# Performance work log

Measured on AMD Instinct MI355X. Metric: run time of the kernel, lower is better.

## Reference

```python
import jax, jax.numpy as jnp
import numpy as np

N = 262144   # number of units (batched instances of the module)
G = 128      # universe_field side length
D = 128      # dimension
RADIUS = 3   # min(3, G//2) == 3

# First D=128 neighborhood offsets in the original triple-loop order (i-major, j, k)
_grid = np.stack(np.meshgrid(np.arange(-RADIUS, RADIUS + 1),
                             np.arange(-RADIUS, RADIUS + 1),
                             np.arange(-RADIUS, RADIUS + 1), indexing='ij'), -1).reshape(-1, 3)[:D]
OI = jnp.asarray(_grid[:, 0], dtype=jnp.int32)
OJ = jnp.asarray(_grid[:, 1], dtype=jnp.int32)
OK = jnp.asarray(_grid[:, 2], dtype=jnp.int32)


def setup_inputs() -> dict:
    key = jax.random.key(0)
    ks = jax.random.split(key, 8)
    return {
        'universe_field': jax.random.normal(ks[0], (G, G, G), jnp.float32),
        'positions': jax.random.uniform(ks[1], (N, 3), jnp.float32) * G,
        'signatures': jax.random.normal(ks[2], (N, D), jnp.float32),
        'offsets': jax.random.normal(ks[3], (N, 3), jnp.float32) * 0.1,
        'W1': jax.random.normal(ks[4], (2 * D, D), jnp.float32) * (1.0 / np.sqrt(2 * D)),
        'b1': jax.random.normal(ks[5], (D,), jnp.float32) * 0.01,
        'W2': jax.random.normal(ks[6], (D, D), jnp.float32) * (1.0 / np.sqrt(D)),
        'b2': jax.random.normal(ks[7], (D,), jnp.float32) * 0.01,
    }


def _sample_local(field, pos):
    # pos: [N,3] float; truncate to int (torch .long()) then clamp, like the original
    pc = jnp.clip(jax.lax.stop_gradient(pos).astype(jnp.int32), 0, G - 1)  # [N,3]
    xx = jnp.clip(pc[:, 0:1] + OI[None, :], 0, G - 1)  # [N,D]
    yy = jnp.clip(pc[:, 1:2] + OJ[None, :], 0, G - 1)
    zz = jnp.clip(pc[:, 2:3] + OK[None, :], 0, G - 1)
    return field[xx, yy, zz]  # [N,D] gathered local field (343 points truncated to D)


def _stability(field, pos, signatures, W1, b1, W2, b2):
    local = _sample_local(field, pos)                       # [N,D]
    combined = jnp.concatenate([signatures, local], axis=-1)  # [N,2D]
    h = jnp.tanh(combined @ W1 + b1)                        # [N,D]
    resp = h @ W2 + b2                                      # [N,D]
    return jnp.linalg.norm(resp - signatures, axis=-1)      # [N]


def reference(universe_field, positions, signatures, offsets, W1, b1, W2, b2):
    stab_old = _stability(universe_field, positions, signatures, W1, b1, W2, b2)
    test_pos = positions + offsets
    stab_new = _stability(universe_field, test_pos, signatures, W1, b1, W2, b2)
    accept = stab_new <= stab_old                           # revert move if new_stab > old_stab
    final_pos = jnp.where(accept[:, None], test_pos, positions)
    stability = jnp.where(accept, stab_new, stab_old)
    return stability, final_pos
```

## Files before the change

kernel.cpp:

```cpp
#include <hip/hip_runtime.h>
#include <hip/hip_bf16.h>

#define NU 262144
#define GG 128
#define PG 134
#define DD 128

typedef __attribute__((ext_vector_type(8))) short short8;
typedef __attribute__((ext_vector_type(4))) float f32x4;

union Frag { short8 s; unsigned u[4]; };

__device__ __forceinline__ unsigned short f2b(float f) {
  union { float f; unsigned u; } v; v.f = f;
  unsigned r = v.u + 0x7fffu + ((v.u >> 16) & 1u);
  return (unsigned short)(r >> 16);
}
__device__ __forceinline__ unsigned cvtpk(float lo, float hi) {
  unsigned r;
  asm("v_cvt_pk_bf16_f32 %0, %1, %2" : "=v"(r) : "v"(lo), "v"(hi));
  return r;
}
__device__ __forceinline__ float unplo(unsigned w) {
  union { unsigned u; float f; } v; v.u = w << 16; return v.f;
}
__device__ __forceinline__ float unphi(unsigned w) {
  union { unsigned u; float f; } v; v.u = w & 0xffff0000u; return v.f;
}

__device__ __forceinline__ float fast_tanh(float x) {
  float e = __expf(fabsf(x) * 2.0f);
  float r = __frcp_rn(e + 1.0f);
  return copysignf(fmaf(-2.0f, r, 1.0f), x);
}

struct alignas(16) RowdT { int v[20]; };
static constexpr RowdT mkrowd() {
  RowdT t{};
  for (int r = 0; r < 20; ++r) {
    int rr = (r < 18) ? r : 18;
    int di = (rr < 18) ? (-3 + rr / 7) : -1;
    int dj = (rr < 18) ? (-3 + rr % 7) : 1;
    t.v[r] = (di * PG + dj) * PG - 3;
  }
  return t;
}
__device__ constexpr RowdT ROWD = mkrowd();

__global__ void prep_field(const float* __restrict__ f, unsigned short* __restrict__ fp) {
  int idx = blockIdx.x * 256 + threadIdx.x;
  if (idx >= PG * PG * PG) return;
  int z = idx % PG, t = idx / PG;
  int y = t % PG, x = t / PG;
  int xx = min(max(x - 3, 0), GG - 1);
  int yy = min(max(y - 3, 0), GG - 1);
  int zz = min(max(z - 3, 0), GG - 1);
  fp[idx] = f2b(f[(xx * GG + yy) * GG + zz]);
}

__global__ void prep_w(const float* __restrict__ W1, const float* __restrict__ W2,
                       unsigned short* __restrict__ wall) {
  int idx = blockIdx.x * 256 + threadIdx.x;
  if (idx >= 6656) return;
  int kt = idx >> 9, nt = (idx >> 6) & 7, ln = idx & 63;
  int n = nt * 16 + (ln & 15), lg = ln >> 4;
  short8 s;
  if (kt < 4) {
    int k0 = kt * 32 + lg * 8;
#pragma unroll
    for (int j = 0; j < 8; ++j) s[j] = (short)f2b(W1[(k0 + j) * DD + n]);
  } else if (kt < 9) {
    int r = (kt - 4) * 4 + lg;
#pragma unroll
    for (int j = 0; j < 8; ++j) {
      bool valid = (r < 18 && j < 7) || (r == 18 && j < 2);
      int row = 128 + ((r < 18) ? (r * 7 + j) : (126 + j));
      s[j] = valid ? (short)f2b(W1[row * DD + n]) : (short)0;
    }
  } else {
    int k0 = (kt - 9) * 32 + lg * 8;
#pragma unroll
    for (int j = 0; j < 8; ++j) s[j] = (short)f2b(W2[(k0 + j) * DD + n]);
  }
  ((short8*)wall)[idx] = s;
}

__global__ __launch_bounds__(512, 4) void atu_main(
    const float* __restrict__ pos, const float* __restrict__ sig,
    const float* __restrict__ offs,
    const float* __restrict__ b1, const float* __restrict__ b2,
    const unsigned short* __restrict__ fpad, const unsigned short* __restrict__ wall,
    float* __restrict__ out_stab, float* __restrict__ out_pos)
{
  __shared__ unsigned short ldsw[2][8192];
  __shared__ alignas(16) unsigned short ns[8][2048];
  const int tid  = threadIdx.x;
  const int lane = tid & 63;
  const int lg   = lane >> 4, lm = lane & 15;
  const int wid  = tid >> 6;
  int bid = blockIdx.x;
  int swz = (bid & 7) * 256 + (bid >> 3);
  const int ub = swz * 128 + wid * 16;
  const int un = ub + lm;
  char* nsb = (char*)&ns[wid][0];

  int abase[2];
  {
    float px = pos[un * 3 + 0], py = pos[un * 3 + 1], pz = pos[un * 3 + 2];
    float qx = px + offs[un * 3 + 0], qy = py + offs[un * 3 + 1], qz = pz + offs[un * 3 + 2];
    int ax = min(max((int)px, 0), GG - 1), ay = min(max((int)py, 0), GG - 1), az = min(max((int)pz, 0), GG - 1);
    int bx = min(max((int)qx, 0), GG - 1), by = min(max((int)qy, 0), GG - 1), bz = min(max((int)qz, 0), GG - 1);
    abase[0] = ((ax + 3) * PG + (ay + 3)) * PG + (az + 3);
    abase[1] = ((bx + 3) * PG + (by + 3)) * PG + (bz + 3);
  }

  const short8* wfr = (const short8*)wall;
  const char* fpadb = (const char*)fpad;

  f32x4 acc[8][2];
#pragma unroll
  for (int nt = 0; nt < 8; ++nt) { acc[nt][0] = f32x4{0.f,0.f,0.f,0.f}; acc[nt][1] = f32x4{0.f,0.f,0.f,0.f}; }
  f32x4 acc2[8][2];
  unsigned Q[2][8][2];

#define WRBUF(H, R0, R1)                                                        \
  *(short8*)((char*)&ldsw[H][0] + tid * 16) = (R0);                             \
  *(short8*)((char*)&ldsw[H][0] + 8192 + tid * 16) = (R1);

#define SIG_KT(KT, HALF)                                                        \
  {                                                                             \
    const f32x4* sp = (const f32x4*)(sig + (size_t)un * DD + (KT) * 32 + lg * 8); \
    f32x4 a = sp[0], b = sp[1];                                                 \
    Frag B;                                                                     \
    B.u[0] = cvtpk(a[0], a[1]); B.u[1] = cvtpk(a[2], a[3]);                     \
    B.u[2] = cvtpk(b[0], b[1]); B.u[3] = cvtpk(b[2], b[3]);                     \
     \
    *(short8*)(nsb + ((KT) * 4 + lg) * 256 + lm * 16) = B.s;                    \
    const char* buf = (const char*)&ldsw[HALF][0] + (((KT) & 1) ? 8192 : 0);    \
    _Pragma("unroll")                                                           \
    for (int nt = 0; nt < 8; ++nt) {                                            \
      short8 af = *(const short8*)(buf + (nt * 64 + lane) * 16);                \
      acc[nt][0] = __builtin_amdgcn_mfma_f32_16x16x32_bf16(af, B.s, acc[nt][0], 0, 0, 0); \
    }                                                                           \
  }

#define ROW_KT(KT, HALF)                                                        \
  {                                                                             \
    int rd = ROWD.v[((KT) - 4) * 4 + lg];                                       \
    short8 B0 = *(const short8*)(fpadb + 2 * (size_t)(abase[0] + rd));          \
    short8 B1 = *(const short8*)(fpadb + 2 * (size_t)(abase[1] + rd));          \
    const char* buf = (const char*)&ldsw[HALF][0] + (((KT) & 1) ? 8192 : 0);    \
    _Pragma("unroll")                                                           \
    for (int nt = 0; nt < 8; ++nt) {                                            \
      short8 af = *(const short8*)(buf + (nt * 64 + lane) * 16);                \
      acc[nt][0] = __builtin_amdgcn_mfma_f32_16x16x32_bf16(af, B0, acc[nt][0], 0, 0, 0); \
      acc[nt][1] = __builtin_amdgcn_mfma_f32_16x16x32_bf16(af, B1, acc[nt][1], 0, 0, 0); \
    }                                                                           \
  }

#define G2_KT(KT, HALF)                                                         \
  {                                                                             \
    constexpr int kb = (KT) - 9;                                                \
    Frag W[2];                                                                  \
    _Pragma("unroll")                                                           \
    for (int ut = 0; ut < 2; ++ut) {                                            \
      int qa0 = (int)Q[ut][2 * kb][0],     qa1 = (int)Q[ut][2 * kb][1];         \
      int qb0 = (int)Q[ut][2 * kb + 1][0], qb1 = (int)Q[ut][2 * kb + 1][1];     \
      int r00 = __builtin_amdgcn_ds_bpermute(ad0, qa0);                         \
      int r01 = __builtin_amdgcn_ds_bpermute(ad0, qa1);                         \
      int r10 = __builtin_amdgcn_ds_bpermute(ad1, qa0);                         \
      int r11 = __builtin_amdgcn_ds_bpermute(ad1, qa1);                         \
      int s00 = __builtin_amdgcn_ds_bpermute(ad0, qb0);                         \
      int s01 = __builtin_amdgcn_ds_bpermute(ad0, qb1);                         \
      int s10 = __builtin_amdgcn_ds_bpermute(ad1, qb0);                         \
      int s11 = __builtin_amdgcn_ds_bpermute(ad1, qb1);                         \
      W[ut].u[0] = (unsigned)(hi ? s00 : r00);                                  \
      W[ut].u[1] = (unsigned)(hi ? s01 : r01);                                  \
      W[ut].u[2] = (unsigned)(hi ? s10 : r10);                                  \
      W[ut].u[3] = (unsigned)(hi ? s11 : r11);                                  \
    }                                                                           \
    const char* buf = (const char*)&ldsw[HALF][0] + (((KT) & 1) ? 8192 : 0);    \
    _Pragma("unroll")                                                           \
    for (int nt = 0; nt < 8; ++nt) {                                            \
      short8 af = *(const short8*)(buf + (nt * 64 + lane) * 16);                \
      acc2[nt][0] = __builtin_amdgcn_mfma_f32_16x16x32_bf16(af, W[0].s, acc2[nt][0], 0, 0, 0); \
      acc2[nt][1] = __builtin_amdgcn_mfma_f32_16x16x32_bf16(af, W[1].s, acc2[nt][1], 0, 0, 0); \
    }                                                                           \
  }

  const int ad0 = ((((2 * lg) & 3) * 16) + lm) * 4;
  const int ad1 = ((((2 * lg + 1) & 3) * 16) + lm) * 4;
  const bool hi = (lg >= 2);

  short8 c0 = wfr[tid],        c1 = wfr[512 + tid];
  short8 n0 = wfr[1024 + tid], n1 = wfr[1536 + tid];
  WRBUF(0, c0, c1)
  __syncthreads();

  c0 = wfr[2048 + tid]; c1 = wfr[2560 + tid];
  SIG_KT(0, 0) SIG_KT(1, 0)
  WRBUF(1, n0, n1)
  __syncthreads();

  n0 = wfr[3072 + tid]; n1 = wfr[3584 + tid];
  SIG_KT(2, 1) SIG_KT(3, 1)
  WRBUF(0, c0, c1)
  __syncthreads();

#pragma unroll
  for (int nt = 0; nt < 8; ++nt) acc[nt][1] = acc[nt][0];

  c0 = wfr[4096 + tid]; c1 = wfr[4608 + tid];
  ROW_KT(4, 0) ROW_KT(5, 0)
  WRBUF(1, n0, n1)
  __syncthreads();

  n0 = wfr[5120 + tid]; n1 = wfr[5632 + tid];
  ROW_KT(6, 1) ROW_KT(7, 1)
  WRBUF(0, c0, c1)
  __syncthreads();

  c0 = wfr[6144 + tid];
  ROW_KT(8, 0)

#pragma unroll
  for (int nt = 0; nt < 8; ++nt) {
    f32x4 b1v = *(const f32x4*)(b1 + nt * 16 + lg * 4);
#pragma unroll
    for (int ut = 0; ut < 2; ++ut) {
      float h0 = fast_tanh(acc[nt][ut][0] + b1v[0]);
      float h1 = fast_tanh(acc[nt][ut][1] + b1v[1]);
      float h2 = fast_tanh(acc[nt][ut][2] + b1v[2]);
      float h3 = fast_tanh(acc[nt][ut][3] + b1v[3]);
      Q[ut][nt][0] = cvtpk(h0, h1);
      Q[ut][nt][1] = cvtpk(h2, h3);
    }
  }
#pragma unroll
  for (int nt = 0; nt < 8; ++nt) {
    f32x4 b2v = *(const f32x4*)(b2 + nt * 16 + lg * 4);
    acc2[nt][0] = b2v; acc2[nt][1] = b2v;
  }

  G2_KT(9, 0)
  WRBUF(1, n0, n1)
  __syncthreads();

  G2_KT(10, 1) G2_KT(11, 1)
  *(short8*)((char*)&ldsw[0][0] + tid * 16) = c0;
  __syncthreads();

  G2_KT(12, 0)

  float ssq[2] = {0.f, 0.f};
#pragma unroll
  for (int nt = 0; nt < 8; ++nt) {
    unsigned long long w64 = *(const unsigned long long*)
        (nsb + (nt * 2 + (lg >> 1)) * 256 + lm * 16 + (lg & 1) * 8);
    unsigned w0 = (unsigned)w64, w1 = (unsigned)(w64 >> 32);
    float sv0 = unplo(w0), sv1 = unphi(w0);
    float sv2 = unplo(w1), sv3 = unphi(w1);
#pragma unroll
    for (int ut = 0; ut < 2; ++ut) {
      float d0 = acc2[nt][ut][0] - sv0;
      float d1 = acc2[nt][ut][1] - sv1;
      float d2 = acc2[nt][ut][2] - sv2;
      float d3 = acc2[nt][ut][3] - sv3;
      ssq[ut] = fmaf(d0, d0, ssq[ut]);
      ssq[ut] = fmaf(d1, d1, ssq[ut]);
      ssq[ut] = fmaf(d2, d2, ssq[ut]);
      ssq[ut] = fmaf(d3, d3, ssq[ut]);
    }
  }
  ssq[0] += __shfl_xor(ssq[0], 16, 64); ssq[0] += __shfl_xor(ssq[0], 32, 64);
  ssq[1] += __shfl_xor(ssq[1], 16, 64); ssq[1] += __shfl_xor(ssq[1], 32, 64);

  if (lane < 16) {
    float px = pos[un * 3 + 0], py = pos[un * 3 + 1], pz = pos[un * 3 + 2];
    float ox = offs[un * 3 + 0], oy = offs[un * 3 + 1], oz = offs[un * 3 + 2];
    bool ok = ssq[1] <= ssq[0];
    out_stab[un] = sqrtf(ok ? ssq[1] : ssq[0]);
    out_pos[un * 3 + 0] = ok ? px + ox : px;
    out_pos[un * 3 + 1] = ok ? py + oy : py;
    out_pos[un * 3 + 2] = ok ? pz + oz : pz;
  }
#undef WRBUF
#undef SIG_KT
#undef ROW_KT
#undef G2_KT
}

extern "C" void kernel_launch(void* const* d_in, const int* in_sizes, int n_in,
                              void* d_out, int out_size, void* d_ws, size_t ws_size,
                              hipStream_t stream) {
  const float* field = (const float*)d_in[0];
  const float* pos   = (const float*)d_in[1];
  const float* sig   = (const float*)d_in[2];
  const float* offs  = (const float*)d_in[3];
  const float* W1    = (const float*)d_in[4];
  const float* b1    = (const float*)d_in[5];
  const float* W2    = (const float*)d_in[6];
  const float* b2    = (const float*)d_in[7];
  float* out_stab = (float*)d_out;
  float* out_pos  = out_stab + NU;

  char* ws = (char*)d_ws;
  unsigned short* fpad = (unsigned short*)ws;
  unsigned short* wall = (unsigned short*)(ws + 4812800);

  prep_field<<<(PG * PG * PG + 255) / 256, 256, 0, stream>>>(field, fpad);
  prep_w<<<26, 256, 0, stream>>>(W1, W2, wall);
  atu_main<<<NU / 128, 512, 0, stream>>>(pos, sig, offs, b1, b2,
                                         fpad, wall, out_stab, out_pos);
}
```

Measured before the change: 147.0 us.

## Stream weights via global_load_lds and software-prefetch signature and field fragments

After: 137.3 us. 1.07x faster.

```diff
diff --git a/kernel.cpp b/kernel.cpp
--- a/kernel.cpp
+++ b/kernel.cpp
@@ -103,6 +103,8 @@
   const int ub = swz * 128 + wid * 16;
   const int un = ub + lm;
   char* nsb = (char*)&ns[wid][0];
+  const char* wallb = (const char*)wall;
+  const char* fpadb = (const char*)fpad;
 
   int abase[2];
   {
@@ -114,124 +116,139 @@
     abase[1] = ((bx + 3) * PG + (by + 3)) * PG + (bz + 3);
   }
 
-  const short8* wfr = (const short8*)wall;
-  const char* fpadb = (const char*)fpad;
+#define GLL2(KTA, H)                                                              \
+  __builtin_amdgcn_global_load_lds(                                               \
+      (const unsigned*)(wallb + (((KTA) * 512 + tid) * 16)),                      \
+      (unsigned*)((char*)&ldsw[H][0] + wid * 1024), 16, 0, 0);                    \
+  __builtin_amdgcn_global_load_lds(                                               \
+      (const unsigned*)(wallb + ((((KTA) + 1) * 512 + tid) * 16)),                \
+      (unsigned*)((char*)&ldsw[H][0] + 8192 + wid * 1024), 16, 0, 0);
+
+#define GLL1(KTA, H)                                                              \
+  __builtin_amdgcn_global_load_lds(                                               \
+      (const unsigned*)(wallb + (((KTA) * 512 + tid) * 16)),                      \
+      (unsigned*)((char*)&ldsw[H][0] + wid * 1024), 16, 0, 0);
+
+  GLL2(0, 0)
+  f32x4 spa = *(const f32x4*)(sig + (size_t)un * DD + lg * 8);
+  f32x4 spb = *(const f32x4*)(sig + (size_t)un * DD + lg * 8 + 4);
+  short8 rAc, rBc;
+  {
+    int rd = ROWD.v[lg];
+    rAc = *(const short8*)(fpadb + 2 * (size_t)(abase[0] + rd));
+    rBc = *(const short8*)(fpadb + 2 * (size_t)(abase[1] + rd));
+  }
 
   f32x4 acc[8][2];
 #pragma unroll
-  for (int nt = 0; nt < 8; ++nt) { acc[nt][0] = f32x4{0.f,0.f,0.f,0.f}; acc[nt][1] = f32x4{0.f,0.f,0.f,0.f}; }
+  for (int nt = 0; nt < 8; ++nt) acc[nt][0] = *(const f32x4*)(b1 + nt * 16 + lg * 4);
   f32x4 acc2[8][2];
   unsigned Q[2][8][2];
 
-#define WRBUF(H, R0, R1)                                                        \
-  *(short8*)((char*)&ldsw[H][0] + tid * 16) = (R0);                             \
-  *(short8*)((char*)&ldsw[H][0] + 8192 + tid * 16) = (R1);
-
-#define SIG_KT(KT, HALF)                                                        \
-  {                                                                             \
-    const f32x4* sp = (const f32x4*)(sig + (size_t)un * DD + (KT) * 32 + lg * 8); \
-    f32x4 a = sp[0], b = sp[1];                                                 \
-    Frag B;                                                                     \
-    B.u[0] = cvtpk(a[0], a[1]); B.u[1] = cvtpk(a[2], a[3]);                     \
-    B.u[2] = cvtpk(b[0], b[1]); B.u[3] = cvtpk(b[2], b[3]);                     \
-     \
-    *(short8*)(nsb + ((KT) * 4 + lg) * 256 + lm * 16) = B.s;                    \
-    const char* buf = (const char*)&ldsw[HALF][0] + (((KT) & 1) ? 8192 : 0);    \
-    _Pragma("unroll")                                                           \
-    for (int nt = 0; nt < 8; ++nt) {                                            \
-      short8 af = *(const short8*)(buf + (nt * 64 + lane) * 16);                \
+  __syncthreads();
+
+#define SIG_KT(KT, HALF)                                                          \
+  {                                                                               \
+    f32x4 na, nb;                                                                 \
+    if ((KT) < 3) {                                                               \
+      na = *(const f32x4*)(sig + (size_t)un * DD + ((KT) + 1) * 32 + lg * 8);     \
+      nb = *(const f32x4*)(sig + (size_t)un * DD + ((KT) + 1) * 32 + lg * 8 + 4); \
+    }                                                                             \
+    Frag B;                                                                       \
+    B.u[0] = cvtpk(spa[0], spa[1]); B.u[1] = cvtpk(spa[2], spa[3]);               \
+    B.u[2] = cvtpk(spb[0], spb[1]); B.u[3] = cvtpk(spb[2], spb[3]);               \
+    *(short8*)(nsb + ((KT) * 4 + lg) * 256 + lm * 16) = B.s;                      \
+    const char* buf = (const char*)&ldsw[HALF][0] + (((KT) & 1) ? 8192 : 0);      \
+    _Pragma("unroll")                                                             \
+    for (int nt = 0; nt < 8; ++nt) {                                              \
+      short8 af = *(const short8*)(buf + (nt * 64 + lane) * 16);                  \
       acc[nt][0] = __builtin_amdgcn_mfma_f32_16x16x32_bf16(af, B.s, acc[nt][0], 0, 0, 0); \
-    }                                                                           \
-  }
-
-#define ROW_KT(KT, HALF)                                                        \
-  {                                                                             \
-    int rd = ROWD.v[((KT) - 4) * 4 + lg];                                       \
-    short8 B0 = *(const short8*)(fpadb + 2 * (size_t)(abase[0] + rd));          \
-    short8 B1 = *(const short8*)(fpadb + 2 * (size_t)(abase[1] + rd));          \
-    const char* buf = (const char*)&ldsw[HALF][0] + (((KT) & 1) ? 8192 : 0);    \
-    _Pragma("unroll")                                                           \
-    for (int nt = 0; nt < 8; ++nt) {                                            \
-      short8 af = *(const short8*)(buf + (nt * 64 + lane) * 16);                \
-      acc[nt][0] = __builtin_amdgcn_mfma_f32_16x16x32_bf16(af, B0, acc[nt][0], 0, 0, 0); \
-      acc[nt][1] = __builtin_amdgcn_mfma_f32_16x16x32_bf16(af, B1, acc[nt][1], 0, 0, 0); \
-    }                                                                           \
-  }
-
-#define G2_KT(KT, HALF)                                                         \
-  {                                                                             \
-    constexpr int kb = (KT) - 9;                                                \
-    Frag W[2];                                                                  \
-    _Pragma("unroll")                                                           \
-    for (int ut = 0; ut < 2; ++ut) {                                            \
-      int qa0 = (int)Q[ut][2 * kb][0],     qa1 = (int)Q[ut][2 * kb][1];         \
-      int qb0 = (int)Q[ut][2 * kb + 1][0], qb1 = (int)Q[ut][2 * kb + 1][1];     \
-      int r00 = __builtin_amdgcn_ds_bpermute(ad0, qa0);                         \
-      int r01 = __builtin_amdgcn_ds_bpermute(ad0, qa1);                         \
-      int r10 = __builtin_amdgcn_ds_bpermute(ad1, qa0);                         \
-      int r11 = __builtin_amdgcn_ds_bpermute(ad1, qa1);                         \
-      int s00 = __builtin_amdgcn_ds_bpermute(ad0, qb0);                         \
-      int s01 = __builtin_amdgcn_ds_bpermute(ad0, qb1);                         \
-      int s10 = __builtin_amdgcn_ds_bpermute(ad1, qb0);                         \
-      int s11 = __builtin_amdgcn_ds_bpermute(ad1, qb1);                         \
-      W[ut].u[0] = (unsigned)(hi ? s00 : r00);                                  \
-      W[ut].u[1] = (unsigned)(hi ? s01 : r01);                                  \
-      W[ut].u[2] = (unsigned)(hi ? s10 : r10);                                  \
-      W[ut].u[3] = (unsigned)(hi ? s11 : r11);                                  \
-    }                                                                           \
-    const char* buf = (const char*)&ldsw[HALF][0] + (((KT) & 1) ? 8192 : 0);    \
-    _Pragma("unroll")                                                           \
-    for (int nt = 0; nt < 8; ++nt) {                                            \
-      short8 af = *(const short8*)(buf + (nt * 64 + lane) * 16);                \
+    }                                                                             \
+    if ((KT) < 3) { spa = na; spb = nb; }                                         \
+  }
+
+#define ROW_KT(KT, HALF)                                                          \
+  {                                                                               \
+    short8 nA, nB;                                                                \
+    if ((KT) < 8) {                                                               \
+      int rn = ROWD.v[((KT) - 3) * 4 + lg];                                       \
+      nA = *(const short8*)(fpadb + 2 * (size_t)(abase[0] + rn));                 \
+      nB = *(const short8*)(fpadb + 2 * (size_t)(abase[1] + rn));                 \
+    }                                                                             \
+    const char* buf = (const char*)&ldsw[HALF][0] + (((KT) & 1) ? 8192 : 0);      \
+    _Pragma("unroll")                                                             \
+    for (int nt = 0; nt < 8; ++nt) {                                              \
+      short8 af = *(const short8*)(buf + (nt * 64 + lane) * 16);                  \
+      acc[nt][0] = __builtin_amdgcn_mfma_f32_16x16x32_bf16(af, rAc, acc[nt][0], 0, 0, 0); \
+      acc[nt][1] = __builtin_amdgcn_mfma_f32_16x16x32_bf16(af, rBc, acc[nt][1], 0, 0, 0); \
+    }                                                                             \
+    if ((KT) < 8) { rAc = nA; rBc = nB; }                                         \
+  }
+
+#define G2_KT(KT, HALF)                                                           \
+  {                                                                               \
+    constexpr int kb = (KT) - 9;                                                  \
+    Frag W[2];                                                                    \
+    _Pragma("unroll")                                                             \
+    for (int ut = 0; ut < 2; ++ut) {                                              \
+      int qa0 = (int)Q[ut][2 * kb][0],     qa1 = (int)Q[ut][2 * kb][1];           \
+      int qb0 = (int)Q[ut][2 * kb + 1][0], qb1 = (int)Q[ut][2 * kb + 1][1];       \
+      int r00 = __builtin_amdgcn_ds_bpermute(ad0, qa0);                           \
+      int r01 = __builtin_amdgcn_ds_bpermute(ad0, qa1);                           \
+      int r10 = __builtin_amdgcn_ds_bpermute(ad1, qa0);                           \
+      int r11 = __builtin_amdgcn_ds_bpermute(ad1, qa1);                           \
+      int s00 = __builtin_amdgcn_ds_bpermute(ad0, qb0);                           \
+      int s01 = __builtin_amdgcn_ds_bpermute(ad0, qb1);                           \
+      int s10 = __builtin_amdgcn_ds_bpermute(ad1, qb0);                           \
+      int s11 = __builtin_amdgcn_ds_bpermute(ad1, qb1);                           \
+      W[ut].u[0] = (unsigned)(hi ? s00 : r00);                                    \
+      W[ut].u[1] = (unsigned)(hi ? s01 : r01);                                    \
+      W[ut].u[2] = (unsigned)(hi ? s10 : r10);                                    \
+      W[ut].u[3] = (unsigned)(hi ? s11 : r11);                                    \
+    }                                                                             \
+    const char* buf = (const char*)&ldsw[HALF][0] + (((KT) & 1) ? 8192 : 0);      \
+    _Pragma("unroll")                                                             \
+    for (int nt = 0; nt < 8; ++nt) {                                              \
+      short8 af = *(const short8*)(buf + (nt * 64 + lane) * 16);                  \
       acc2[nt][0] = __builtin_amdgcn_mfma_f32_16x16x32_bf16(af, W[0].s, acc2[nt][0], 0, 0, 0); \
       acc2[nt][1] = __builtin_amdgcn_mfma_f32_16x16x32_bf16(af, W[1].s, acc2[nt][1], 0, 0, 0); \
-    }                                                                           \
+    }                                                                             \
   }
 
   const int ad0 = ((((2 * lg) & 3) * 16) + lm) * 4;
   const int ad1 = ((((2 * lg + 1) & 3) * 16) + lm) * 4;
   const bool hi = (lg >= 2);
 
-  short8 c0 = wfr[tid],        c1 = wfr[512 + tid];
-  short8 n0 = wfr[1024 + tid], n1 = wfr[1536 + tid];
-  WRBUF(0, c0, c1)
-  __syncthreads();
-
-  c0 = wfr[2048 + tid]; c1 = wfr[2560 + tid];
+  GLL2(2, 1)
   SIG_KT(0, 0) SIG_KT(1, 0)
-  WRBUF(1, n0, n1)
-  __syncthreads();
-
-  n0 = wfr[3072 + tid]; n1 = wfr[3584 + tid];
+  __syncthreads();
+
+  GLL2(4, 0)
   SIG_KT(2, 1) SIG_KT(3, 1)
-  WRBUF(0, c0, c1)
   __syncthreads();
 
 #pragma unroll
   for (int nt = 0; nt < 8; ++nt) acc[nt][1] = acc[nt][0];
 
-  c0 = wfr[4096 + tid]; c1 = wfr[4608 + tid];
+  GLL2(6, 1)
   ROW_KT(4, 0) ROW_KT(5, 0)
-  WRBUF(1, n0, n1)
-  __syncthreads();
-
-  n0 = wfr[5120 + tid]; n1 = wfr[5632 + tid];
+  __syncthreads();
+
+  GLL2(8, 0)
   ROW_KT(6, 1) ROW_KT(7, 1)
-  WRBUF(0, c0, c1)
-  __syncthreads();
-
-  c0 = wfr[6144 + tid];
+  __syncthreads();
+
+  GLL2(10, 1)
   ROW_KT(8, 0)
 
 #pragma unroll
   for (int nt = 0; nt < 8; ++nt) {
-    f32x4 b1v = *(const f32x4*)(b1 + nt * 16 + lg * 4);
 #pragma unroll
     for (int ut = 0; ut < 2; ++ut) {
-      float h0 = fast_tanh(acc[nt][ut][0] + b1v[0]);
-      float h1 = fast_tanh(acc[nt][ut][1] + b1v[1]);
-      float h2 = fast_tanh(acc[nt][ut][2] + b1v[2]);
-      float h3 = fast_tanh(acc[nt][ut][3] + b1v[3]);
+      float h0 = fast_tanh(acc[nt][ut][0]);
+      float h1 = fast_tanh(acc[nt][ut][1]);
+      float h2 = fast_tanh(acc[nt][ut][2]);
+      float h3 = fast_tanh(acc[nt][ut][3]);
       Q[ut][nt][0] = cvtpk(h0, h1);
       Q[ut][nt][1] = cvtpk(h2, h3);
     }
@@ -243,11 +260,10 @@
   }
 
   G2_KT(9, 0)
-  WRBUF(1, n0, n1)
-  __syncthreads();
-
+  __syncthreads();
+
+  GLL1(12, 0)
   G2_KT(10, 1) G2_KT(11, 1)
-  *(short8*)((char*)&ldsw[0][0] + tid * 16) = c0;
   __syncthreads();
 
   G2_KT(12, 0)
@@ -284,7 +300,8 @@
     out_pos[un * 3 + 1] = ok ? py + oy : py;
     out_pos[un * 3 + 2] = ok ? pz + oz : pz;
   }
-#undef WRBUF
+#undef GLL2
+#undef GLL1
 #undef SIG_KT
 #undef ROW_KT
 #undef G2_KT
```
